# Performance work log

Measured on AMD Instinct MI355X. Metric: run time of the kernel, lower is better.

Reference implementation:

```python
import jax, jax.numpy as jnp
import numpy as np

B, T, D, M = 64, 2048, 256, 20
UNIT = 2
RADIUS_FACTOR = 0.2
SIGMA_FACTOR = 0.2
KERNEL = 3
TOPK = 100
EPS = 1e-12


def setup_inputs() -> dict:
    key = jax.random.key(0)
    ks = jax.random.split(key, 10)
    x = jax.random.normal(ks[0], (B, T, D), jnp.float32)
    saliency = jax.random.normal(ks[1], (B, T), jnp.float32)
    # ground-truth boundaries in frame units, -1 start marks padding objects
    b0 = jax.random.uniform(ks[2], (B, M), minval=0.0, maxval=UNIT * (T - 100))
    length = jax.random.uniform(ks[3], (B, M), minval=UNIT * 2.0, maxval=UNIT * 100.0)
    b1 = jnp.minimum(b0 + length, float(UNIT * T))
    valid = jax.random.uniform(ks[4], (B, M)) < 0.8
    b0 = jnp.where(valid, b0, -1.0)
    boundary = jnp.stack([b0, b1], axis=-1)
    sc = 1.0 / np.sqrt(D)
    w_center = jax.random.normal(ks[5], (D, 1), jnp.float32) * sc
    w_window = jax.random.normal(ks[6], (D, 1), jnp.float32) * sc
    w_offset = jax.random.normal(ks[7], (D, 1), jnp.float32) * sc
    zb = jnp.zeros((1,), jnp.float32)
    return dict(x=x, w_center=w_center, b_center=zb, w_window=w_window, b_window=zb,
                w_offset=w_offset, b_offset=zb, saliency=saliency, boundary=boundary)


def _get_targets(boundary):
    # boundary: [B, M, 2] in frame units; vectorized version of the torch double loop
    b0 = boundary[..., 0]
    b1 = boundary[..., 1]
    valid = b0 != -1.0                                   # [B, M]
    b0c = b0 / UNIT
    b1c = (b1 - UNIT) / UNIT
    centers = jnp.minimum((b0c + b1c) * 0.5, T - 0.5)    # [B, M]
    windows = b1c - b0c                                   # [B, M]
    radius = (windows * RADIUS_FACTOR).astype(jnp.int32)  # trunc like .int()
    sigma = (radius.astype(jnp.float32) + 1.0) * SIGMA_FACTOR
    ci = centers.astype(jnp.int32)                        # [B, M]
    t = jnp.arange(T)
    d = t[None, None, :] - ci[..., None]                  # [B, M, T]
    g = jnp.exp(-(d.astype(jnp.float32) ** 2) / (2.0 * sigma[..., None] ** 2))
    inband = (jnp.abs(d) <= radius[..., None]) & valid[..., None]
    g = jnp.where(inband, g, 0.0)
    center_tgt = g.max(axis=1)                            # scatter-max over objects
    rows = jnp.arange(B)[:, None]
    idx = jnp.where(valid, ci, T)                         # out-of-range -> dropped
    z = jnp.zeros((B, T), jnp.float32)
    window_tgt = z.at[rows, idx].set(windows, mode='drop')
    offset_tgt = z.at[rows, idx].set(centers - ci.astype(jnp.float32), mode='drop')
    weight = z.at[rows, idx].set(1.0, mode='drop')
    avg_factor = valid.sum().astype(jnp.float32)
    return center_tgt, window_tgt, offset_tgt, weight, avg_factor


def _get_boundary(center_pred, window_pred, offset_pred):
    pad = (KERNEL - 1) // 2
    hmax = jax.lax.reduce_window(center_pred, -jnp.inf, jax.lax.max,
                                 (1, KERNEL), (1, 1), [(0, 0), (pad, pad)])
    cp = jnp.where(hmax == center_pred, center_pred, 0.0)
    scores, inds = jax.lax.top_k(cp, TOPK)                # [B, TOPK]
    off = jnp.maximum(jnp.take_along_axis(offset_pred, inds, axis=1), 0.0)
    center = inds.astype(jnp.float32) + off
    window = jnp.maximum(jnp.take_along_axis(window_pred, inds, axis=1), 0.0)
    lo = jnp.clip(center - window / 2, 0.0, T - 1.0) * UNIT
    hi = jnp.clip(center + window / 2, 0.0, T - 1.0) * UNIT + UNIT
    return jnp.stack([lo, hi, scores], axis=-1)           # [B, TOPK, 3]


def reference(x, w_center, b_center, w_window, b_window, w_offset, b_offset, saliency, boundary):
    mask = (saliency >= 0).astype(x.dtype)                # [B, T]
    center_pred = jax.nn.sigmoid(jnp.einsum('btd,do->bt', x, w_center) + b_center[0]) * mask
    window_pred = jnp.einsum('btd,do->bt', x, w_window) + b_window[0]
    offset_pred = jnp.einsum('btd,do->bt', x, w_offset) + b_offset[0]

    center_tgt, window_tgt, offset_tgt, weight, avg = _get_targets(boundary)

    # GaussianFocalLoss (alpha=2, gamma=4), weighted by mask, mean over avg_factor
    pos = (center_tgt == 1.0).astype(jnp.float32)
    pos_loss = -jnp.log(center_pred + EPS) * (1.0 - center_pred) ** 2 * pos
    neg_loss = -jnp.log(1.0 - center_pred + EPS) * center_pred ** 2 * (1.0 - center_tgt) ** 4
    center_loss = ((pos_loss + neg_loss) * mask).sum() / avg
    window_loss = 0.1 * (jnp.abs(window_pred - window_tgt) * weight).sum() / avg
    offset_loss = 1.0 * (jnp.abs(offset_pred - offset_tgt) * weight).sum() / avg

    boundary_out = _get_boundary(center_pred, window_pred, offset_pred)
    return (boundary_out, center_loss, window_loss, offset_loss)
```

## Files before the change

kernel.cpp:

```cpp
#include <hip/hip_runtime.h>
#include <math.h>

#define BB 64
#define TT 2048
#define DD 256
#define MM 20
#define TOPK_N 100
#define EPSF 1e-12f

__global__ __launch_bounds__(256) void preds_kernel(
    const float* __restrict__ x,
    const float* __restrict__ wc, const float* __restrict__ bc,
    const float* __restrict__ ww, const float* __restrict__ bw,
    const float* __restrict__ wo, const float* __restrict__ bo,
    const float* __restrict__ sal,
    float* __restrict__ cp, float* __restrict__ wp, float* __restrict__ op,
    unsigned int* __restrict__ ticket)
{
    if (blockIdx.x == 0 && threadIdx.x == 0) *ticket = 0u;

    const int lane = threadIdx.x & 63;
    const int sub  = lane >> 4;
    const int cg   = lane & 15;
    const int waveg  = blockIdx.x * 4 + (threadIdx.x >> 6);
    const int nwaves = gridDim.x * 4;

    float4 wc4[4], ww4[4], wo4[4];
    #pragma unroll
    for (int k = 0; k < 4; ++k) {
        wc4[k] = ((const float4*)wc)[k * 16 + cg];
        ww4[k] = ((const float4*)ww)[k * 16 + cg];
        wo4[k] = ((const float4*)wo)[k * 16 + cg];
    }
    const float bcs = bc[0], bws = bw[0], bos = bo[0];

    const int ngroups = BB * TT / 4;
    for (int g = waveg; g < ngroups; g += nwaves) {
        const int row = g * 4 + sub;
        const float4* xr = (const float4*)(x + (size_t)row * DD);
        float sc = 0.0f, sw = 0.0f, so = 0.0f;
        #pragma unroll
        for (int k = 0; k < 4; ++k) {
            const float4 x4 = xr[k * 16 + cg];
            sc += x4.x * wc4[k].x + x4.y * wc4[k].y + x4.z * wc4[k].z + x4.w * wc4[k].w;
            sw += x4.x * ww4[k].x + x4.y * ww4[k].y + x4.z * ww4[k].z + x4.w * ww4[k].w;
            so += x4.x * wo4[k].x + x4.y * wo4[k].y + x4.z * wo4[k].z + x4.w * wo4[k].w;
        }
        #pragma unroll
        for (int m = 8; m >= 1; m >>= 1) {
            sc += __shfl_xor(sc, m, 64);
            sw += __shfl_xor(sw, m, 64);
            so += __shfl_xor(so, m, 64);
        }
        if (cg == 0) {
            const float mask = (sal[row] >= 0.0f) ? 1.0f : 0.0f;
            const float s = 1.0f / (1.0f + expf(-(sc + bcs)));
            cp[row] = s * mask;
            wp[row] = sw + bws;
            op[row] = so + bos;
        }
    }
}

__global__ __launch_bounds__(256) void fused_kernel(
    const float* __restrict__ boundary, const float* __restrict__ sal,
    const float* __restrict__ cp, const float* __restrict__ wp,
    const float* __restrict__ op, float* __restrict__ partials,
    unsigned int* __restrict__ ticket, float* __restrict__ out)
{
    __shared__ int   s_ci[MM];
    __shared__ float s_win[MM], s_off[MM], s_sig[MM];
    __shared__ int   s_rad[MM], s_valid[MM], s_last[MM];
    __shared__ float s_red[4][4];
    __shared__ unsigned long long keys[TT];
    __shared__ unsigned long long cand[TT];
    __shared__ int s_nz;
    __shared__ int s_islast;

    const int b = blockIdx.x;
    const int tid = threadIdx.x;
    const float* row = cp + b * TT;

    if (tid == 0) s_nz = 0;
    if (tid < MM) {
        const float b0 = boundary[(b * MM + tid) * 2 + 0];
        const float b1 = boundary[(b * MM + tid) * 2 + 1];
        const int v = (b0 != -1.0f) ? 1 : 0;
        const float b0c = b0 * 0.5f;
        const float b1c = (b1 - 2.0f) * 0.5f;
        const float c = fminf((b0c + b1c) * 0.5f, (float)TT - 0.5f);
        const float w = b1c - b0c;
        const int r = (int)(w * 0.2f);
        const float sg = ((float)r + 1.0f) * 0.2f;
        const int ci = (int)c;
        s_ci[tid] = ci; s_win[tid] = w; s_off[tid] = c - (float)ci;
        s_sig[tid] = sg; s_rad[tid] = r; s_valid[tid] = v;
    }
    __syncthreads();
    if (tid < MM) {
        int last = s_valid[tid];
        if (last) {
            for (int m2 = tid + 1; m2 < MM; ++m2)
                if (s_valid[m2] && s_ci[m2] == s_ci[tid]) { last = 0; break; }
        }
        s_last[tid] = last;
    }
    __syncthreads();

    float cl = 0.0f, wl = 0.0f, ol = 0.0f, cnt = 0.0f;
    if (tid < MM) {
        if (s_valid[tid]) cnt = 1.0f;
        if (s_last[tid]) {
            const int t = s_ci[tid];
            wl = fabsf(wp[b * TT + t] - s_win[tid]);
            ol = fabsf(op[b * TT + t] - s_off[tid]);
        }
    }
    for (int t = tid; t < TT; t += 256) {
        const float p = row[t];
        const float l = (t > 0) ? row[t - 1] : -1.0f;
        const float r = (t < TT - 1) ? row[t + 1] : -1.0f;
        const float hm = fmaxf(p, fmaxf(l, r));
        const float v = (hm == p) ? p : 0.0f;
        const unsigned long long key =
            ((unsigned long long)__float_as_uint(v) << 32)
          | (unsigned int)(0xFFFFFFFFu - (unsigned int)t);
        keys[t] = key;
        if (v != 0.0f) {
            const int pos = atomicAdd(&s_nz, 1);
            cand[pos] = key;
        }
        float ctgt = 0.0f;
        for (int m = 0; m < MM; ++m) {
            if (!s_valid[m]) continue;
            const int d = t - s_ci[m];
            const int ad = d < 0 ? -d : d;
            if (ad <= s_rad[m]) {
                const float df = (float)d;
                const float sg = s_sig[m];
                const float g = expf(-(df * df) / (2.0f * sg * sg));
                ctgt = fmaxf(ctgt, g);
            }
        }
        const float mask = (sal[b * TT + t] >= 0.0f) ? 1.0f : 0.0f;
        const float pos = (ctgt == 1.0f) ? 1.0f : 0.0f;
        const float om = 1.0f - p;
        const float pl = -logf(p + EPSF) * om * om * pos;
        const float q = 1.0f - ctgt;
        const float q2 = q * q;
        const float nl = -logf(1.0f - p + EPSF) * p * p * (q2 * q2);
        cl += (pl + nl) * mask;
    }
    #pragma unroll
    for (int m = 32; m >= 1; m >>= 1) {
        cl  += __shfl_xor(cl,  m, 64);
        wl  += __shfl_xor(wl,  m, 64);
        ol  += __shfl_xor(ol,  m, 64);
        cnt += __shfl_xor(cnt, m, 64);
    }
    if ((tid & 63) == 0) {
        const int w = tid >> 6;
        s_red[w][0] = cl; s_red[w][1] = wl; s_red[w][2] = ol; s_red[w][3] = cnt;
    }
    __syncthreads();
    if (tid == 0) {
        float a = 0, b2 = 0, c = 0, d = 0;
        for (int w = 0; w < 4; ++w) {
            a += s_red[w][0]; b2 += s_red[w][1]; c += s_red[w][2]; d += s_red[w][3];
        }
        partials[b * 4 + 0] = a; partials[b * 4 + 1] = b2;
        partials[b * 4 + 2] = c; partials[b * 4 + 3] = d;
    }

    const int nz = s_nz;
    unsigned long long* arr;
    int n;
    if (nz >= TOPK_N) {
        n = 128;
        while (n < nz) n <<= 1;
        for (int i = nz + tid; i < n; i += 256) cand[i] = 0ull;
        arr = cand;
    } else {
        n = TT;
        arr = keys;
    }
    __syncthreads();
    for (int k = 2; k <= n; k <<= 1) {
        for (int j = k >> 1; j >= 1; j >>= 1) {
            for (int i = tid; i < n; i += 256) {
                const int p = i ^ j;
                if (p > i) {
                    const bool desc = ((i & k) == 0);
                    const unsigned long long a = arr[i], bk = arr[p];
                    const bool sw = desc ? (a < bk) : (a > bk);
                    if (sw) { arr[i] = bk; arr[p] = a; }
                }
            }
            __syncthreads();
        }
    }

    if (tid < TOPK_N) {
        const unsigned long long kk = arr[tid];
        const int idx = (int)(0xFFFFFFFFu - (unsigned int)kk);
        const float score = __uint_as_float((unsigned int)(kk >> 32));
        const float off = fmaxf(op[b * TT + idx], 0.0f);
        const float center = (float)idx + off;
        const float win = fmaxf(wp[b * TT + idx], 0.0f);
        const float lo = fminf(fmaxf(center - win * 0.5f, 0.0f), (float)TT - 1.0f) * 2.0f;
        const float hi = fminf(fmaxf(center + win * 0.5f, 0.0f), (float)TT - 1.0f) * 2.0f + 2.0f;
        float* o = out + (b * TOPK_N + tid) * 3;
        o[0] = lo; o[1] = hi; o[2] = score;
    }

    __threadfence();
    if (tid == 0) {
        const unsigned int prev = atomicAdd(ticket, 1u);
        s_islast = (prev == (unsigned int)(BB - 1)) ? 1 : 0;
    }
    __syncthreads();
    if (s_islast) {
        __threadfence();
        if (tid < 64) {
            const volatile float* pp = (const volatile float*)partials;
            float fcl  = pp[tid * 4 + 0];
            float fwl  = pp[tid * 4 + 1];
            float fol  = pp[tid * 4 + 2];
            float fcnt = pp[tid * 4 + 3];
            #pragma unroll
            for (int m = 32; m >= 1; m >>= 1) {
                fcl  += __shfl_xor(fcl,  m, 64);
                fwl  += __shfl_xor(fwl,  m, 64);
                fol  += __shfl_xor(fol,  m, 64);
                fcnt += __shfl_xor(fcnt, m, 64);
            }
            if (tid == 0) {
                out[BB * TOPK_N * 3 + 0] = fcl / fcnt;
                out[BB * TOPK_N * 3 + 1] = 0.1f * fwl / fcnt;
                out[BB * TOPK_N * 3 + 2] = fol / fcnt;
            }
        }
    }
}

extern "C" void kernel_launch(void* const* d_in, const int* in_sizes, int n_in,
                              void* d_out, int out_size, void* d_ws, size_t ws_size,
                              hipStream_t stream) {
    const float* x   = (const float*)d_in[0];
    const float* wc  = (const float*)d_in[1];
    const float* bc  = (const float*)d_in[2];
    const float* ww  = (const float*)d_in[3];
    const float* bw  = (const float*)d_in[4];
    const float* wo  = (const float*)d_in[5];
    const float* bo  = (const float*)d_in[6];
    const float* sal = (const float*)d_in[7];
    const float* bnd = (const float*)d_in[8];
    float* out = (float*)d_out;

    float* ws = (float*)d_ws;
    float* cp = ws;
    float* wp = ws + BB * TT;
    float* op = ws + 2 * BB * TT;
    float* partials = ws + 3 * BB * TT;
    unsigned int* ticket = (unsigned int*)(ws + 3 * BB * TT + 4 * BB);

    preds_kernel<<<2048, 256, 0, stream>>>(x, wc, bc, ww, bw, wo, bo, sal,
                                           cp, wp, op, ticket);
    fused_kernel<<<BB, 256, 0, stream>>>(bnd, sal, cp, wp, op, partials, ticket, out);
}
```

Baseline: 256.2 us.

## Fuse projection and per-batch loss/topk into one kernel via per-batch tickets

Merges the projection kernel and the per-batch loss/top-k kernel into a single launch. Each block computes 64 rows of predictions, then takes a per-batch atomic ticket, and the last of the 32 blocks for a batch runs the loss, peak-detection and bitonic sort stage. This removes the second kernel launch and lets early batches' tail work overlap with projection of later batches. It also merges the two shared key buffers into one, recomputing keys only in the rare fallback path, and adds a memset launch to reset the tickets.

```diff
diff --git a/kernel.cpp b/kernel.cpp
--- a/kernel.cpp
+++ b/kernel.cpp
@@ -8,80 +8,83 @@
 #define TOPK_N 100
 #define EPSF 1e-12f
 
-__global__ __launch_bounds__(256) void preds_kernel(
+__global__ __launch_bounds__(256) void mono_kernel(
     const float* __restrict__ x,
     const float* __restrict__ wc, const float* __restrict__ bc,
     const float* __restrict__ ww, const float* __restrict__ bw,
     const float* __restrict__ wo, const float* __restrict__ bo,
-    const float* __restrict__ sal,
+    const float* __restrict__ sal, const float* __restrict__ boundary,
     float* __restrict__ cp, float* __restrict__ wp, float* __restrict__ op,
-    unsigned int* __restrict__ ticket)
+    float* __restrict__ partials, unsigned int* __restrict__ ticket,
+    float* __restrict__ out)
 {
-    if (blockIdx.x == 0 && threadIdx.x == 0) *ticket = 0u;
-
-    const int lane = threadIdx.x & 63;
-    const int sub  = lane >> 4;
-    const int cg   = lane & 15;
-    const int waveg  = blockIdx.x * 4 + (threadIdx.x >> 6);
-    const int nwaves = gridDim.x * 4;
-
-    float4 wc4[4], ww4[4], wo4[4];
-    #pragma unroll
-    for (int k = 0; k < 4; ++k) {
-        wc4[k] = ((const float4*)wc)[k * 16 + cg];
-        ww4[k] = ((const float4*)ww)[k * 16 + cg];
-        wo4[k] = ((const float4*)wo)[k * 16 + cg];
-    }
-    const float bcs = bc[0], bws = bw[0], bos = bo[0];
-
-    const int ngroups = BB * TT / 4;
-    for (int g = waveg; g < ngroups; g += nwaves) {
-        const int row = g * 4 + sub;
-        const float4* xr = (const float4*)(x + (size_t)row * DD);
-        float sc = 0.0f, sw = 0.0f, so = 0.0f;
-        #pragma unroll
-        for (int k = 0; k < 4; ++k) {
-            const float4 x4 = xr[k * 16 + cg];
-            sc += x4.x * wc4[k].x + x4.y * wc4[k].y + x4.z * wc4[k].z + x4.w * wc4[k].w;
-            sw += x4.x * ww4[k].x + x4.y * ww4[k].y + x4.z * ww4[k].z + x4.w * ww4[k].w;
-            so += x4.x * wo4[k].x + x4.y * wo4[k].y + x4.z * wo4[k].z + x4.w * wo4[k].w;
-        }
-        #pragma unroll
-        for (int m = 8; m >= 1; m >>= 1) {
-            sc += __shfl_xor(sc, m, 64);
-            sw += __shfl_xor(sw, m, 64);
-            so += __shfl_xor(so, m, 64);
-        }
-        if (cg == 0) {
-            const float mask = (sal[row] >= 0.0f) ? 1.0f : 0.0f;
-            const float s = 1.0f / (1.0f + expf(-(sc + bcs)));
-            cp[row] = s * mask;
-            wp[row] = sw + bws;
-            op[row] = so + bos;
-        }
-    }
-}
-
-__global__ __launch_bounds__(256) void fused_kernel(
-    const float* __restrict__ boundary, const float* __restrict__ sal,
-    const float* __restrict__ cp, const float* __restrict__ wp,
-    const float* __restrict__ op, float* __restrict__ partials,
-    unsigned int* __restrict__ ticket, float* __restrict__ out)
-{
+    __shared__ unsigned long long buf[TT];
     __shared__ int   s_ci[MM];
     __shared__ float s_win[MM], s_off[MM], s_sig[MM];
     __shared__ int   s_rad[MM], s_valid[MM], s_last[MM];
     __shared__ float s_red[4][4];
-    __shared__ unsigned long long keys[TT];
-    __shared__ unsigned long long cand[TT];
     __shared__ int s_nz;
+    __shared__ int s_consumer;
     __shared__ int s_islast;
 
-    const int b = blockIdx.x;
-    const int tid = threadIdx.x;
+    const int blk  = blockIdx.x;
+    const int tid  = threadIdx.x;
+    const int lane = tid & 63;
+    const int sub  = lane >> 4;
+    const int cg   = lane & 15;
+    const int wv   = tid >> 6;
+    const int b    = blk >> 5;
+
+    {
+        float4 wc4[4], ww4[4], wo4[4];
+        #pragma unroll
+        for (int k = 0; k < 4; ++k) {
+            wc4[k] = ((const float4*)wc)[k * 16 + cg];
+            ww4[k] = ((const float4*)ww)[k * 16 + cg];
+            wo4[k] = ((const float4*)wo)[k * 16 + cg];
+        }
+        const float bcs = bc[0], bws = bw[0], bos = bo[0];
+
+        for (int g = blk * 16 + wv; g < blk * 16 + 16; g += 4) {
+            const int row = g * 4 + sub;
+            const float4* xr = (const float4*)(x + (size_t)row * DD);
+            float sc = 0.0f, sw = 0.0f, so = 0.0f;
+            #pragma unroll
+            for (int k = 0; k < 4; ++k) {
+                const float4 x4 = xr[k * 16 + cg];
+                sc += x4.x * wc4[k].x + x4.y * wc4[k].y + x4.z * wc4[k].z + x4.w * wc4[k].w;
+                sw += x4.x * ww4[k].x + x4.y * ww4[k].y + x4.z * ww4[k].z + x4.w * ww4[k].w;
+                so += x4.x * wo4[k].x + x4.y * wo4[k].y + x4.z * wo4[k].z + x4.w * wo4[k].w;
+            }
+            #pragma unroll
+            for (int m = 8; m >= 1; m >>= 1) {
+                sc += __shfl_xor(sc, m, 64);
+                sw += __shfl_xor(sw, m, 64);
+                so += __shfl_xor(so, m, 64);
+            }
+            if (cg == 0) {
+                const float mask = (sal[row] >= 0.0f) ? 1.0f : 0.0f;
+                const float s = 1.0f / (1.0f + expf(-(sc + bcs)));
+                cp[row] = s * mask;
+                wp[row] = sw + bws;
+                op[row] = so + bos;
+            }
+        }
+    }
+    __syncthreads();
+
+    if (tid == 0) {
+        __threadfence();
+        const unsigned int prev = atomicAdd(&ticket[b], 1u);
+        s_consumer = (prev == 31u) ? 1 : 0;
+        s_nz = 0;
+    }
+    __syncthreads();
+    if (!s_consumer) return;
+    __threadfence();
+
     const float* row = cp + b * TT;
 
-    if (tid == 0) s_nz = 0;
     if (tid < MM) {
         const float b0 = boundary[(b * MM + tid) * 2 + 0];
         const float b1 = boundary[(b * MM + tid) * 2 + 1];
@@ -125,10 +128,9 @@
         const unsigned long long key =
             ((unsigned long long)__float_as_uint(v) << 32)
           | (unsigned int)(0xFFFFFFFFu - (unsigned int)t);
-        keys[t] = key;
         if (v != 0.0f) {
             const int pos = atomicAdd(&s_nz, 1);
-            cand[pos] = key;
+            buf[pos] = key;
         }
         float ctgt = 0.0f;
         for (int m = 0; m < MM; ++m) {
@@ -171,18 +173,25 @@
         partials[b * 4 + 0] = a; partials[b * 4 + 1] = b2;
         partials[b * 4 + 2] = c; partials[b * 4 + 3] = d;
     }
+    __syncthreads();
 
     const int nz = s_nz;
-    unsigned long long* arr;
     int n;
     if (nz >= TOPK_N) {
         n = 128;
         while (n < nz) n <<= 1;
-        for (int i = nz + tid; i < n; i += 256) cand[i] = 0ull;
-        arr = cand;
+        for (int i = nz + tid; i < n; i += 256) buf[i] = 0ull;
     } else {
         n = TT;
-        arr = keys;
+        for (int t = tid; t < TT; t += 256) {
+            const float p = row[t];
+            const float l = (t > 0) ? row[t - 1] : -1.0f;
+            const float r = (t < TT - 1) ? row[t + 1] : -1.0f;
+            const float hm = fmaxf(p, fmaxf(l, r));
+            const float v = (hm == p) ? p : 0.0f;
+            buf[t] = ((unsigned long long)__float_as_uint(v) << 32)
+                   | (unsigned int)(0xFFFFFFFFu - (unsigned int)t);
+        }
     }
     __syncthreads();
     for (int k = 2; k <= n; k <<= 1) {
@@ -191,9 +200,9 @@
                 const int p = i ^ j;
                 if (p > i) {
                     const bool desc = ((i & k) == 0);
-                    const unsigned long long a = arr[i], bk = arr[p];
+                    const unsigned long long a = buf[i], bk = buf[p];
                     const bool sw = desc ? (a < bk) : (a > bk);
-                    if (sw) { arr[i] = bk; arr[p] = a; }
+                    if (sw) { buf[i] = bk; buf[p] = a; }
                 }
             }
             __syncthreads();
@@ -201,7 +210,7 @@
     }
 
     if (tid < TOPK_N) {
-        const unsigned long long kk = arr[tid];
+        const unsigned long long kk = buf[tid];
         const int idx = (int)(0xFFFFFFFFu - (unsigned int)kk);
         const float score = __uint_as_float((unsigned int)(kk >> 32));
         const float off = fmaxf(op[b * TT + idx], 0.0f);
@@ -215,7 +224,7 @@
 
     __threadfence();
     if (tid == 0) {
-        const unsigned int prev = atomicAdd(ticket, 1u);
+        const unsigned int prev = atomicAdd(&ticket[BB], 1u);
         s_islast = (prev == (unsigned int)(BB - 1)) ? 1 : 0;
     }
     __syncthreads();
@@ -264,7 +273,7 @@
     float* partials = ws + 3 * BB * TT;
     unsigned int* ticket = (unsigned int*)(ws + 3 * BB * TT + 4 * BB);
 
-    preds_kernel<<<2048, 256, 0, stream>>>(x, wc, bc, ww, bw, wo, bo, sal,
-                                           cp, wp, op, ticket);
-    fused_kernel<<<BB, 256, 0, stream>>>(bnd, sal, cp, wp, op, partials, ticket, out);
+    hipMemsetAsync(ticket, 0, (BB + 1) * sizeof(unsigned int), stream);
+    mono_kernel<<<2048, 256, 0, stream>>>(x, wc, bc, ww, bw, wo, bo, sal, bnd,
+                                          cp, wp, op, partials, ticket, out);
 }
```

Result: slower. 390.0 us (+52.2%).
